# Kernel tuning notes

Hardware: AMD Instinct MI355X
Metric: run time of the kernel (lower is better)

## Reference

```python
import jax, jax.numpy as jnp
import numpy as np
import math


def setup_inputs() -> dict:
    key = jax.random.key(0)
    ks = jax.random.split(key, 8)
    B, L, d_model, d_state, d_conv, expand = 2, 512, 1024, 64, 4, 2
    d_inner = expand * d_model  # 2048
    x = jax.random.normal(ks[0], (B, L, d_model), jnp.float32)
    in_proj_w = jax.random.normal(ks[1], (d_model, 2 * d_inner), jnp.float32) * (d_model ** -0.5)
    conv_w = jax.random.normal(ks[2], (d_inner, 1, d_conv), jnp.float32) * (d_conv ** -0.5)
    conv_b = jnp.zeros((d_inner,), jnp.float32)
    x_proj_w = jax.random.normal(ks[3], (d_inner, 2 * d_state + 1), jnp.float32) * (d_inner ** -0.5)
    dt_w = jax.random.normal(ks[4], (1, d_inner), jnp.float32)
    # dt bias init: softplus^{-1} of dt ~ LogUniform(dt_min, dt_max)
    dt = jnp.exp(jax.random.uniform(ks[5], (d_inner,)) * (math.log(0.1) - math.log(0.001)) + math.log(0.001))
    dt_b = dt + jnp.log(-jnp.expm1(-dt))
    A_log = jnp.broadcast_to(jnp.log(jnp.arange(1, d_state + 1, dtype=jnp.float32)), (d_inner, d_state)) + 0.0
    D = jnp.ones((d_inner,), jnp.float32)
    out_proj_w = jax.random.normal(ks[6], (d_inner, d_model), jnp.float32) * (d_inner ** -0.5)
    return {"x": x, "in_proj_w": in_proj_w, "conv_w": conv_w, "conv_b": conv_b,
            "x_proj_w": x_proj_w, "dt_w": dt_w, "dt_b": dt_b, "A_log": A_log,
            "D": D, "out_proj_w": out_proj_w}


def _mamba_forward(x, in_proj_w, conv_w, conv_b, x_proj_w, dt_w, dt_b, A_log, D, out_proj_w):
    Bsz, L, _ = x.shape
    d_inner, _, K = conv_w.shape
    d_state = A_log.shape[1]
    # in_proj -> split into x-branch and gate z
    xz = x @ in_proj_w                       # (B, L, 2*d_inner)
    xs, z = jnp.split(xz, 2, axis=-1)
    # depthwise causal conv1d (pad K-1 on the left == torch pad both + truncate to L)
    xc = jax.lax.conv_general_dilated(
        xs.transpose(0, 2, 1), conv_w, (1,), [(K - 1, 0)],
        dimension_numbers=("NCH", "OIH", "NCH"), feature_group_count=d_inner)
    xc = xc + conv_b[None, :, None]
    xs = jax.nn.silu(xc.transpose(0, 2, 1))  # (B, L, d_inner)
    # input-dependent SSM params
    xp = xs @ x_proj_w                       # (B, L, 2*d_state + 1)
    Bm = xp[..., :d_state]                   # (B, L, N)
    Cm = xp[..., d_state:2 * d_state]        # (B, L, N)
    dt_raw = xp[..., -1:]                    # (B, L, 1)
    dt = jax.nn.softplus(dt_raw @ dt_w + dt_b)  # (B, L, d_inner)
    A = -jnp.exp(A_log)                      # (d_inner, N)

    def step(state, inp):
        x_t, B_t, C_t, dt_t = inp            # (B,d), (B,N), (B,N), (B,d)
        dA = jnp.exp(dt_t[..., None] * A)    # (B, d, N)
        state = dA * state + (dt_t * x_t)[..., None] * B_t[:, None, :]
        y = jnp.einsum("bdn,bn->bd", state, C_t) + D * x_t
        return state, y

    init = jnp.zeros((Bsz, d_inner, d_state), xs.dtype)
    seq = (xs.transpose(1, 0, 2), Bm.transpose(1, 0, 2),
           Cm.transpose(1, 0, 2), dt.transpose(1, 0, 2))
    new_state, ys = jax.lax.scan(step, init, seq)
    y = ys.transpose(1, 0, 2)                # (B, L, d_inner)
    y = y * jax.nn.silu(z)
    out = y @ out_proj_w                     # (B, L, d_model)
    return out, new_state


def reference(x, in_proj_w, conv_w, conv_b, x_proj_w, dt_w, dt_b, A_log, D, out_proj_w):
    return _mamba_forward(x, in_proj_w, conv_w, conv_b, x_proj_w, dt_w, dt_b, A_log, D, out_proj_w)
```

## Files before the change

kernel.cpp:

```cpp
#include <hip/hip_runtime.h>
#include <hip/hip_bf16.h>


#define N_TOK   1024
#define SEQ_L   512
#define D_MODEL 1024
#define D_INNER 2048
#define D_STATE 64
#define D_XZ    4096
#define N_XP    129

typedef __attribute__((ext_vector_type(8))) short bf16x8;
typedef __attribute__((ext_vector_type(4))) float f32x4;

__device__ __forceinline__ unsigned short f2bf(float f) {
  __hip_bfloat16 h = __float2bfloat16(f);
  return *reinterpret_cast<unsigned short*>(&h);
}
__device__ __forceinline__ float bf16lo(unsigned int u) { return __uint_as_float(u << 16); }
__device__ __forceinline__ float bf16hi(unsigned int u) { return __uint_as_float(u & 0xffff0000u); }

__global__ __launch_bounds__(256) void transpose_bf16(
    const float* __restrict__ src, __hip_bfloat16* __restrict__ dst, int R, int C) {
  __shared__ float t[64][65];
  int c0 = blockIdx.x * 64, r0 = blockIdx.y * 64;
  int tc = threadIdx.x & 63, tg = threadIdx.x >> 6;
#pragma unroll
  for (int i = 0; i < 16; ++i) {
    int r = r0 + tg + i * 4, c = c0 + tc;
    t[tg + i * 4][tc] = (r < R && c < C) ? src[(size_t)r * C + c] : 0.f;
  }
  __syncthreads();
#pragma unroll
  for (int i = 0; i < 16; ++i) {
    int c = c0 + tg + i * 4, r = r0 + tc;
    if (c < C && r < R) dst[(size_t)c * R + r] = __float2bfloat16(t[tc][tg + i * 4]);
  }
}

__global__ __launch_bounds__(256) void convert_bf16(
    const float* __restrict__ src, __hip_bfloat16* __restrict__ dst, int n) {
  int i = blockIdx.x * 256 + threadIdx.x;
  if (i < n) dst[i] = __float2bfloat16(src[i]);
}

template<int BM>
__global__ __launch_bounds__(256) void gemm_bf16_tn(
    const __hip_bfloat16* __restrict__ A, const __hip_bfloat16* __restrict__ Bt,
    float* __restrict__ C, int M, int N, int K) {
  const int MF = BM / 32;
  __shared__ short As[BM][40];
  __shared__ short Bs[128][40];
  const int brow = blockIdx.y * BM, bcol = blockIdx.x * 128;
  const int tid = threadIdx.x;
  const int lane = tid & 63, wave = tid >> 6;
  const int wm = wave >> 1, wn = wave & 1;
  const int l15 = lane & 15, lk = lane >> 4;
  f32x4 acc[MF][4] = {};
  for (int k0 = 0; k0 < K; k0 += 32) {
#pragma unroll
    for (int i = 0; i < BM / 64; ++i) {
      int v = tid + i * 256;
      int r = v >> 2, kc = (v & 3) * 8;
      *(bf16x8*)((char*)&As[0][0] + r * 80 + kc * 2) =
          *(const bf16x8*)&A[(size_t)(brow + r) * K + k0 + kc];
    }
#pragma unroll
    for (int i = 0; i < 2; ++i) {
      int v = tid + i * 256;
      int r = v >> 2, kc = (v & 3) * 8;
      *(bf16x8*)((char*)&Bs[0][0] + r * 80 + kc * 2) =
          *(const bf16x8*)&Bt[(size_t)(bcol + r) * K + k0 + kc];
    }
    __syncthreads();
    bf16x8 af[MF], bfr[4];
#pragma unroll
    for (int m = 0; m < MF; ++m)
      af[m] = *(const bf16x8*)((const char*)&As[0][0] + (wm * (BM / 2) + m * 16 + l15) * 80 + lk * 16);
#pragma unroll
    for (int n = 0; n < 4; ++n)
      bfr[n] = *(const bf16x8*)((const char*)&Bs[0][0] + (wn * 64 + n * 16 + l15) * 80 + lk * 16);
#pragma unroll
    for (int m = 0; m < MF; ++m)
#pragma unroll
      for (int n = 0; n < 4; ++n)
        acc[m][n] = __builtin_amdgcn_mfma_f32_16x16x32_bf16(af[m], bfr[n], acc[m][n], 0, 0, 0);
    __syncthreads();
  }
#pragma unroll
  for (int m = 0; m < MF; ++m) {
    int row = brow + wm * (BM / 2) + m * 16 + lk * 4;
#pragma unroll
    for (int n = 0; n < 4; ++n) {
      int col = bcol + wn * 64 + n * 16 + l15;
#pragma unroll
      for (int r = 0; r < 4; ++r)
        C[(size_t)(row + r) * N + col] = acc[m][n][r];
    }
  }
}

template<int BM>
__global__ __launch_bounds__(256) void gemm_splitk(
    const __hip_bfloat16* __restrict__ A, const __hip_bfloat16* __restrict__ Bt,
    float* __restrict__ P, int M, int N, int K, int kchunk) {
  const int MF = BM / 32;
  __shared__ short As[BM][40];
  __shared__ short Bs[128][40];
  const int brow = blockIdx.y * BM, bcol = blockIdx.x * 128;
  const int kbase = blockIdx.z * kchunk;
  const int tid = threadIdx.x;
  const int lane = tid & 63, wave = tid >> 6;
  const int wm = wave >> 1, wn = wave & 1;
  const int l15 = lane & 15, lk = lane >> 4;
  f32x4 acc[MF][4] = {};
  for (int k0 = kbase; k0 < kbase + kchunk; k0 += 32) {
#pragma unroll
    for (int i = 0; i < BM / 64; ++i) {
      int v = tid + i * 256;
      int r = v >> 2, kc = (v & 3) * 8;
      *(bf16x8*)((char*)&As[0][0] + r * 80 + kc * 2) =
          *(const bf16x8*)&A[(size_t)(brow + r) * K + k0 + kc];
    }
#pragma unroll
    for (int i = 0; i < 2; ++i) {
      int v = tid + i * 256;
      int r = v >> 2, kc = (v & 3) * 8;
      bf16x8 bv = {};
      if ((bcol + r) < N)
        bv = *(const bf16x8*)&Bt[(size_t)(bcol + r) * K + k0 + kc];
      *(bf16x8*)((char*)&Bs[0][0] + r * 80 + kc * 2) = bv;
    }
    __syncthreads();
    bf16x8 af[MF], bfr[4];
#pragma unroll
    for (int m = 0; m < MF; ++m)
      af[m] = *(const bf16x8*)((const char*)&As[0][0] + (wm * (BM / 2) + m * 16 + l15) * 80 + lk * 16);
#pragma unroll
    for (int n = 0; n < 4; ++n)
      bfr[n] = *(const bf16x8*)((const char*)&Bs[0][0] + (wn * 64 + n * 16 + l15) * 80 + lk * 16);
#pragma unroll
    for (int m = 0; m < MF; ++m)
#pragma unroll
      for (int n = 0; n < 4; ++n)
        acc[m][n] = __builtin_amdgcn_mfma_f32_16x16x32_bf16(af[m], bfr[n], acc[m][n], 0, 0, 0);
    __syncthreads();
  }
  float* Pz = P + (size_t)blockIdx.z * M * N;
#pragma unroll
  for (int m = 0; m < MF; ++m) {
    int row = brow + wm * (BM / 2) + m * 16 + lk * 4;
#pragma unroll
    for (int n = 0; n < 4; ++n) {
      int col = bcol + wn * 64 + n * 16 + l15;
      if (col < N) {
#pragma unroll
        for (int r = 0; r < 4; ++r)
          Pz[(size_t)(row + r) * N + col] = acc[m][n][r];
      }
    }
  }
}

template<int Z>
__global__ __launch_bounds__(256) void reduce_z(
    const float* __restrict__ P, float* __restrict__ out, int n) {
  int i = (blockIdx.x * 256 + threadIdx.x) * 4;
  if (i >= n) return;
  float4 s = *(const float4*)&P[i];
#pragma unroll
  for (int z = 1; z < Z; ++z) {
    float4 v = *(const float4*)&P[(size_t)z * n + i];
    s.x += v.x; s.y += v.y; s.z += v.z; s.w += v.w;
  }
  *(float4*)&out[i] = s;
}

__global__ __launch_bounds__(256) void reduce_bc(
    const float* __restrict__ P, float4* __restrict__ bcq,
    float* __restrict__ dtr) {
  int tok = blockIdx.x * 8 + (threadIdx.x >> 5);
  int ln = threadIdx.x & 31;
  const float* p0 = P + (size_t)tok * N_XP;
  float b0 = 0.f, b1 = 0.f, c0 = 0.f, c1 = 0.f;
#pragma unroll
  for (int z = 0; z < 16; ++z) {
    const float* pz = p0 + (size_t)z * N_TOK * N_XP;
    b0 += pz[ln]; b1 += pz[ln + 32];
    c0 += pz[64 + ln]; c1 += pz[64 + ln + 32];
  }
  bcq[(size_t)tok * 32 + ln] = make_float4(b0, b1, c0, c1);
  if (ln == 0) {
    float sd = 0.f;
    const float* pd = p0 + 128;
#pragma unroll
    for (int z = 0; z < 16; ++z) sd += pd[(size_t)z * N_TOK * N_XP];
    dtr[tok] = sd;
  }
}

__global__ __launch_bounds__(256) void conv_silu_kernel(
    const float* __restrict__ xz, const float* __restrict__ cw,
    const float* __restrict__ cb, float* __restrict__ xc,
    __hip_bfloat16* __restrict__ xcb) {
  int idx = blockIdx.x * 256 + threadIdx.x;
  int c = idx & (D_INNER - 1);
  int tok = idx >> 11;
  int l = tok & (SEQ_L - 1);
  float acc = cb[c];
#pragma unroll
  for (int k = 0; k < 4; ++k) {
    int ll = l - 3 + k;
    if (ll >= 0) acc = fmaf(xz[(size_t)(tok - 3 + k) * D_XZ + c], cw[c * 4 + k], acc);
  }
  float v = acc / (1.f + __expf(-acc));
  xc[idx] = v;
  xcb[idx] = __float2bfloat16(v);
}

__global__ __launch_bounds__(256) void pack_kernel(
    const float* __restrict__ xzf, const float* __restrict__ xc,
    const float* __restrict__ dtr, const float* __restrict__ dt_w,
    const float* __restrict__ dt_b, const float* __restrict__ Dv,
    float2* __restrict__ uaT, unsigned int* __restrict__ ug2) {
  __shared__ float2 la[64][33];
  int tok0 = blockIdx.x * 32, d0 = blockIdx.y * 64;
  int t = threadIdx.x;
  int dl = t & 63, tc = t >> 6;
  int d = d0 + dl;
  float w = dt_w[d], bb = dt_b[d], Dd = Dv[d];
#pragma unroll
  for (int p = 0; p < 8; ++p) {
    int tl = p * 4 + tc;
    int tok = tok0 + tl;
    float xt = xc[(size_t)tok * D_INNER + d];
    float z = xzf[(size_t)tok * D_XZ + D_INNER + d];
    float dt = dtr[tok] * w + bb;
    dt = (dt > 20.f) ? dt : log1pf(__expf(dt));
    la[dl][tl] = make_float2(dt, dt * xt);
    float g = z / (1.f + __expf(-z));
    ug2[(size_t)tok * D_INNER + d] =
        (unsigned int)f2bf(Dd * xt) | ((unsigned int)f2bf(g) << 16);
  }
  __syncthreads();
  int tl2 = t & 31, dg = t >> 5;
#pragma unroll
  for (int q = 0; q < 8; ++q) {
    int dl2 = q * 8 + dg;
    uaT[(size_t)(d0 + dl2) * N_TOK + tok0 + tl2] = la[dl2][tl2];
  }
}

__global__ __launch_bounds__(256) void gate_kernel(
    const float* __restrict__ praw, const unsigned int* __restrict__ ug2,
    __hip_bfloat16* __restrict__ ybb) {
  __shared__ float tile[64][65];
  int tok0 = blockIdx.x * 64, d0 = blockIdx.y * 64;
  int t = threadIdx.x, tc = t & 63, tg = t >> 6;
#pragma unroll
  for (int i = 0; i < 16; ++i) {
    int dl = tg + i * 4;
    tile[dl][tc] = praw[(size_t)(d0 + dl) * N_TOK + tok0 + tc];
  }
  __syncthreads();
#pragma unroll
  for (int i = 0; i < 16; ++i) {
    int tl = tg + i * 4;
    size_t idx = (size_t)(tok0 + tl) * D_INNER + d0 + tc;
    unsigned u = ug2[idx];
    float v = (tile[tc][tl] + bf16lo(u)) * bf16hi(u);
    ybb[idx] = __float2bfloat16(v);
  }
}

template<int CTRL>
__device__ __forceinline__ float dppadd(float v) {
  int t = __builtin_amdgcn_update_dpp(0, __float_as_int(v), CTRL, 0xF, 0xF, true);
  return v + __int_as_float(t);
}
__device__ __forceinline__ float wave_sum32(float v) {
  v = dppadd<0x111>(v);
  v = dppadd<0x112>(v);
  v = dppadd<0x114>(v);
  v = dppadd<0x118>(v);
  v = dppadd<0x142>(v);
  return v;
}

__global__ __launch_bounds__(256) void scan_fused(
    const float2* __restrict__ uaT, const float4* __restrict__ bcq,
    const float* __restrict__ A_log, float* __restrict__ praw,
    float* __restrict__ state_out) {
  __shared__ float lP[8][64], lS[8][64];
  int bd = blockIdx.x;
  int d = bd & (D_INNER - 1), b = bd >> 11;
  int tid = threadIdx.x;
  int wave = tid >> 6, lane = tid & 63;
  int h = lane >> 5, ln = lane & 31;
  int ch = wave * 2 + h;
  int n0 = ln, n1 = ln + 32;
  const float LOG2E = 1.4426950408889634f;
  float a2_0 = -__expf(A_log[d * D_STATE + n0]) * LOG2E;
  float a2_1 = -__expf(A_log[d * D_STATE + n1]) * LOG2E;
  int tok0 = b * SEQ_L + ch * 64;
  const float2* u0 = uaT + (size_t)d * N_TOK + tok0;
  const float4* q0 = bcq + (size_t)tok0 * 32 + ln;

  float s0 = 0.f, s1 = 0.f, P0 = 1.f, P1 = 1.f;
  {
    const float2* u = u0; const float4* q = q0;
#pragma unroll 1
    for (int t8 = 0; t8 < 8; ++t8) {
#pragma unroll
      for (int j = 0; j < 8; ++j) {
        float2 uv = u[j];
        float4 qv = q[j * 32];
        float dA0 = exp2f(uv.x * a2_0);
        float dA1 = exp2f(uv.x * a2_1);
        P0 *= dA0; P1 *= dA1;
        s0 = fmaf(dA0, s0, uv.y * qv.x);
        s1 = fmaf(dA1, s1, uv.y * qv.y);
      }
      u += 8; q += 256;
    }
  }
  lP[ch][n0] = P0; lP[ch][n1] = P1;
  lS[ch][n0] = s0; lS[ch][n1] = s1;
  __syncthreads();
  float si0 = 0.f, si1 = 0.f;
#pragma unroll
  for (int c = 0; c < 7; ++c) {
    if (c < ch) {
      si0 = fmaf(lP[c][n0], si0, lS[c][n0]);
      si1 = fmaf(lP[c][n1], si1, lS[c][n1]);
    }
  }
  if (ch == 7) {
    state_out[(size_t)bd * D_STATE + n0] = fmaf(P0, si0, s0);
    state_out[(size_t)bd * D_STATE + n1] = fmaf(P1, si1, s1);
  }

  s0 = si0; s1 = si1;
  {
    const float2* u = u0; const float4* q = q0;
    float* po = praw + (size_t)d * N_TOK + tok0;
#pragma unroll 1
    for (int t8 = 0; t8 < 8; ++t8) {
      float pb[8];
#pragma unroll
      for (int j = 0; j < 8; ++j) {
        float2 uv = u[j];
        float4 qv = q[j * 32];
        float dA0 = exp2f(uv.x * a2_0);
        float dA1 = exp2f(uv.x * a2_1);
        s0 = fmaf(dA0, s0, uv.y * qv.x);
        s1 = fmaf(dA1, s1, uv.y * qv.y);
        float p = s0 * qv.z;
        p = fmaf(s1, qv.w, p);
        pb[j] = wave_sum32(p);
      }
      if (ln == 31) {
        *(float4*)(po + t8 * 8) = make_float4(pb[0], pb[1], pb[2], pb[3]);
        *(float4*)(po + t8 * 8 + 4) = make_float4(pb[4], pb[5], pb[6], pb[7]);
      }
      u += 8; q += 256;
    }
  }
}

extern "C" void kernel_launch(void* const* d_in, const int* in_sizes, int n_in,
                              void* d_out, int out_size, void* d_ws, size_t ws_size,
                              hipStream_t stream) {
  const float* x         = (const float*)d_in[0];
  const float* in_proj_w = (const float*)d_in[1];
  const float* conv_w    = (const float*)d_in[2];
  const float* conv_b    = (const float*)d_in[3];
  const float* x_proj_w  = (const float*)d_in[4];
  const float* dt_w      = (const float*)d_in[5];
  const float* dt_b      = (const float*)d_in[6];
  const float* A_log     = (const float*)d_in[7];
  const float* Dvec      = (const float*)d_in[8];
  const float* out_proj_w= (const float*)d_in[9];

  char* w = (char*)d_ws;
  __hip_bfloat16* Wt1 = (__hip_bfloat16*)w; w += (size_t)D_XZ * D_MODEL * 2;
  __hip_bfloat16* Wt2 = (__hip_bfloat16*)w; w += (size_t)N_XP * D_INNER * 2;
  __hip_bfloat16* Wt3 = (__hip_bfloat16*)w; w += (size_t)D_MODEL * D_INNER * 2;
  __hip_bfloat16* xb  = (__hip_bfloat16*)w; w += (size_t)N_TOK * D_MODEL * 2;
  float*          xzf = (float*)w;          w += (size_t)N_TOK * D_XZ * 4;
  float*          xc  = (float*)w;          w += (size_t)N_TOK * D_INNER * 4;
  __hip_bfloat16* xcb = (__hip_bfloat16*)w; w += (size_t)N_TOK * D_INNER * 2;
  float*          P   = (float*)w;          w += (size_t)16 * N_TOK * N_XP * 4;
  float4*         bcq = (float4*)w;         w += (size_t)N_TOK * 32 * 16;
  float*          dtr = (float*)w;          w += (size_t)N_TOK * 4;
  float2*         uaT = (float2*)w;         w += (size_t)D_INNER * N_TOK * 8;
  unsigned int*   ug2 = (unsigned int*)w;   w += (size_t)N_TOK * D_INNER * 4;
  float*          praw = P;
  __hip_bfloat16* ybb  = xcb;
  float*          Pg   = xzf;

  float* out       = (float*)d_out;
  float* state_out = out + (size_t)N_TOK * D_MODEL;

  dim3 blk(256);
  transpose_bf16<<<dim3(D_XZ / 64, D_MODEL / 64), blk, 0, stream>>>(in_proj_w, Wt1, D_MODEL, D_XZ);
  transpose_bf16<<<dim3((N_XP + 63) / 64, D_INNER / 64), blk, 0, stream>>>(x_proj_w, Wt2, D_INNER, N_XP);
  transpose_bf16<<<dim3(D_MODEL / 64, D_INNER / 64), blk, 0, stream>>>(out_proj_w, Wt3, D_INNER, D_MODEL);
  convert_bf16<<<(N_TOK * D_MODEL) / 256, blk, 0, stream>>>(x, xb, N_TOK * D_MODEL);
  gemm_bf16_tn<64><<<dim3(D_XZ / 128, N_TOK / 64), blk, 0, stream>>>(xb, Wt1, xzf, N_TOK, D_XZ, D_MODEL);
  conv_silu_kernel<<<(N_TOK * D_INNER) / 256, blk, 0, stream>>>(xzf, conv_w, conv_b, xc, xcb);
  gemm_splitk<64><<<dim3((N_XP + 127) / 128, N_TOK / 64, 16), blk, 0, stream>>>(xcb, Wt2, P, N_TOK, N_XP, D_INNER, 128);
  reduce_bc<<<N_TOK / 8, blk, 0, stream>>>(P, bcq, dtr);
  pack_kernel<<<dim3(N_TOK / 32, D_INNER / 64), blk, 0, stream>>>(xzf, xc, dtr, dt_w, dt_b, Dvec, uaT, ug2);
  scan_fused<<<2 * D_INNER, blk, 0, stream>>>(uaT, bcq, A_log, praw, state_out);
  gate_kernel<<<dim3(N_TOK / 64, D_INNER / 64), blk, 0, stream>>>(praw, ug2, ybb);
  gemm_splitk<64><<<dim3(D_MODEL / 128, N_TOK / 64, 4), blk, 0, stream>>>(ybb, Wt3, Pg, N_TOK, D_MODEL, D_INNER, 512);
  reduce_z<4><<<(N_TOK * D_MODEL) / 1024, blk, 0, stream>>>(Pg, out, N_TOK * D_MODEL);
}
```

Measured before the change: 300.4 us.

## Fuse weight prep launches and split scan into 16 chunks of 16-lane groups

Merges the three weight transposes and the input bf16 conversion into one prep kernel, with vectorized conversion, to cut launch overhead. The scan is restructured so each thread owns four state elements and works in 16-lane groups, with 16 sequence chunks of 32 tokens per block instead of 8 chunks of 64. B and C are stored as separate float4 arrays to match the new lane layout. This halves the serial chunk length and shortens the per-token reduction to four DPP steps. In exchange it raises per-thread register use and lengthens the serial cross-chunk combine.

```diff
diff --git a/kernel.cpp b/kernel.cpp
--- a/kernel.cpp
+++ b/kernel.cpp
@@ -20,10 +20,30 @@
 __device__ __forceinline__ float bf16lo(unsigned int u) { return __uint_as_float(u << 16); }
 __device__ __forceinline__ float bf16hi(unsigned int u) { return __uint_as_float(u & 0xffff0000u); }
 
-__global__ __launch_bounds__(256) void transpose_bf16(
-    const float* __restrict__ src, __hip_bfloat16* __restrict__ dst, int R, int C) {
+__global__ __launch_bounds__(256) void prep_kernel(
+    const float* __restrict__ w1, const float* __restrict__ w2,
+    const float* __restrict__ w3, const float* __restrict__ x,
+    __hip_bfloat16* __restrict__ Wt1, __hip_bfloat16* __restrict__ Wt2,
+    __hip_bfloat16* __restrict__ Wt3, __hip_bfloat16* __restrict__ xb) {
+  int bid = blockIdx.x;
+  if (bid >= 1632) {
+    int base = (bid - 1632) * 16384 + threadIdx.x * 4;
+#pragma unroll
+    for (int p = 0; p < 16; ++p) {
+      int i = base + p * 1024;
+      float4 v = *(const float4*)&x[i];
+      unsigned lo = (unsigned)f2bf(v.x) | ((unsigned)f2bf(v.y) << 16);
+      unsigned hi = (unsigned)f2bf(v.z) | ((unsigned)f2bf(v.w) << 16);
+      *(uint2*)&xb[i] = make_uint2(lo, hi);
+    }
+    return;
+  }
   __shared__ float t[64][65];
-  int c0 = blockIdx.x * 64, r0 = blockIdx.y * 64;
+  const float* src; __hip_bfloat16* dst; int R, C, cx, t0;
+  if (bid < 1024)      { src = w1; dst = Wt1; R = D_MODEL; C = D_XZ;   cx = 64; t0 = bid; }
+  else if (bid < 1120) { src = w2; dst = Wt2; R = D_INNER; C = N_XP;   cx = 3;  t0 = bid - 1024; }
+  else                 { src = w3; dst = Wt3; R = D_INNER; C = D_MODEL; cx = 16; t0 = bid - 1120; }
+  int c0 = (t0 % cx) * 64, r0 = (t0 / cx) * 64;
   int tc = threadIdx.x & 63, tg = threadIdx.x >> 6;
 #pragma unroll
   for (int i = 0; i < 16; ++i) {
@@ -36,12 +56,6 @@
     int c = c0 + tg + i * 4, r = r0 + tc;
     if (c < C && r < R) dst[(size_t)c * R + r] = __float2bfloat16(t[tc][tg + i * 4]);
   }
-}
-
-__global__ __launch_bounds__(256) void convert_bf16(
-    const float* __restrict__ src, __hip_bfloat16* __restrict__ dst, int n) {
-  int i = blockIdx.x * 256 + threadIdx.x;
-  if (i < n) dst[i] = __float2bfloat16(src[i]);
 }
 
 template<int BM>
@@ -177,24 +191,24 @@
 }
 
 __global__ __launch_bounds__(256) void reduce_bc(
-    const float* __restrict__ P, float4* __restrict__ bcq,
-    float* __restrict__ dtr) {
-  int tok = blockIdx.x * 8 + (threadIdx.x >> 5);
-  int ln = threadIdx.x & 31;
+    const float* __restrict__ P, float4* __restrict__ Bq,
+    float4* __restrict__ Cq, float* __restrict__ dtr) {
+  int tok = blockIdx.x * 16 + (threadIdx.x >> 4);
+  int lq = threadIdx.x & 15;
   const float* p0 = P + (size_t)tok * N_XP;
-  float b0 = 0.f, b1 = 0.f, c0 = 0.f, c1 = 0.f;
+  float b0 = 0, b1 = 0, b2 = 0, b3 = 0, c0 = 0, c1 = 0, c2 = 0, c3 = 0;
 #pragma unroll
   for (int z = 0; z < 16; ++z) {
     const float* pz = p0 + (size_t)z * N_TOK * N_XP;
-    b0 += pz[ln]; b1 += pz[ln + 32];
-    c0 += pz[64 + ln]; c1 += pz[64 + ln + 32];
-  }
-  bcq[(size_t)tok * 32 + ln] = make_float4(b0, b1, c0, c1);
-  if (ln == 0) {
+    b0 += pz[lq];      b1 += pz[lq + 16]; b2 += pz[lq + 32]; b3 += pz[lq + 48];
+    c0 += pz[64 + lq]; c1 += pz[80 + lq]; c2 += pz[96 + lq]; c3 += pz[112 + lq];
+  }
+  Bq[(size_t)tok * 16 + lq] = make_float4(b0, b1, b2, b3);
+  Cq[(size_t)tok * 16 + lq] = make_float4(c0, c1, c2, c3);
+  if (lq == 0) {
     float sd = 0.f;
-    const float* pd = p0 + 128;
-#pragma unroll
-    for (int z = 0; z < 16; ++z) sd += pd[(size_t)z * N_TOK * N_XP];
+#pragma unroll
+    for (int z = 0; z < 16; ++z) sd += p0[(size_t)z * N_TOK * N_XP + 128];
     dtr[tok] = sd;
   }
 }
@@ -278,92 +292,104 @@
   int t = __builtin_amdgcn_update_dpp(0, __float_as_int(v), CTRL, 0xF, 0xF, true);
   return v + __int_as_float(t);
 }
-__device__ __forceinline__ float wave_sum32(float v) {
+__device__ __forceinline__ float qsum16(float v) {
   v = dppadd<0x111>(v);
   v = dppadd<0x112>(v);
   v = dppadd<0x114>(v);
   v = dppadd<0x118>(v);
-  v = dppadd<0x142>(v);
   return v;
 }
 
 __global__ __launch_bounds__(256) void scan_fused(
-    const float2* __restrict__ uaT, const float4* __restrict__ bcq,
-    const float* __restrict__ A_log, float* __restrict__ praw,
-    float* __restrict__ state_out) {
-  __shared__ float lP[8][64], lS[8][64];
+    const float2* __restrict__ uaT, const float4* __restrict__ Bq,
+    const float4* __restrict__ Cq, const float* __restrict__ A_log,
+    float* __restrict__ praw, float* __restrict__ state_out) {
+  __shared__ float lP[16][64], lS[16][64];
   int bd = blockIdx.x;
   int d = bd & (D_INNER - 1), b = bd >> 11;
   int tid = threadIdx.x;
   int wave = tid >> 6, lane = tid & 63;
-  int h = lane >> 5, ln = lane & 31;
-  int ch = wave * 2 + h;
-  int n0 = ln, n1 = ln + 32;
-  const float LOG2E = 1.4426950408889634f;
-  float a2_0 = -__expf(A_log[d * D_STATE + n0]) * LOG2E;
-  float a2_1 = -__expf(A_log[d * D_STATE + n1]) * LOG2E;
-  int tok0 = b * SEQ_L + ch * 64;
+  int qw = lane >> 4, lq = lane & 15;
+  int ch = wave * 4 + qw;
+  const float L2E = 1.4426950408889634f;
+  float a20 = -__expf(A_log[d * D_STATE + lq]) * L2E;
+  float a21 = -__expf(A_log[d * D_STATE + lq + 16]) * L2E;
+  float a22 = -__expf(A_log[d * D_STATE + lq + 32]) * L2E;
+  float a23 = -__expf(A_log[d * D_STATE + lq + 48]) * L2E;
+  int tok0 = b * SEQ_L + ch * 32;
   const float2* u0 = uaT + (size_t)d * N_TOK + tok0;
-  const float4* q0 = bcq + (size_t)tok0 * 32 + ln;
-
-  float s0 = 0.f, s1 = 0.f, P0 = 1.f, P1 = 1.f;
+  const float4* B0 = Bq + (size_t)tok0 * 16 + lq;
+  const float4* C0 = Cq + (size_t)tok0 * 16 + lq;
+
+  float s0 = 0, s1 = 0, s2 = 0, s3 = 0, P0 = 1, P1 = 1, P2 = 1, P3 = 1;
   {
-    const float2* u = u0; const float4* q = q0;
+    const float2* u = u0; const float4* pB = B0;
 #pragma unroll 1
-    for (int t8 = 0; t8 < 8; ++t8) {
+    for (int t8 = 0; t8 < 4; ++t8) {
 #pragma unroll
       for (int j = 0; j < 8; ++j) {
         float2 uv = u[j];
-        float4 qv = q[j * 32];
-        float dA0 = exp2f(uv.x * a2_0);
-        float dA1 = exp2f(uv.x * a2_1);
-        P0 *= dA0; P1 *= dA1;
-        s0 = fmaf(dA0, s0, uv.y * qv.x);
-        s1 = fmaf(dA1, s1, uv.y * qv.y);
+        float4 bv = pB[j * 16];
+        float e0 = exp2f(uv.x * a20), e1 = exp2f(uv.x * a21);
+        float e2 = exp2f(uv.x * a22), e3 = exp2f(uv.x * a23);
+        P0 *= e0; P1 *= e1; P2 *= e2; P3 *= e3;
+        s0 = fmaf(e0, s0, uv.y * bv.x);
+        s1 = fmaf(e1, s1, uv.y * bv.y);
+        s2 = fmaf(e2, s2, uv.y * bv.z);
+        s3 = fmaf(e3, s3, uv.y * bv.w);
       }
-      u += 8; q += 256;
-    }
-  }
-  lP[ch][n0] = P0; lP[ch][n1] = P1;
-  lS[ch][n0] = s0; lS[ch][n1] = s1;
+      u += 8; pB += 128;
+    }
+  }
+  lP[ch][lq] = P0; lP[ch][lq + 16] = P1; lP[ch][lq + 32] = P2; lP[ch][lq + 48] = P3;
+  lS[ch][lq] = s0; lS[ch][lq + 16] = s1; lS[ch][lq + 32] = s2; lS[ch][lq + 48] = s3;
   __syncthreads();
-  float si0 = 0.f, si1 = 0.f;
-#pragma unroll
-  for (int c = 0; c < 7; ++c) {
+  float si0 = 0, si1 = 0, si2 = 0, si3 = 0;
+#pragma unroll
+  for (int c = 0; c < 15; ++c) {
     if (c < ch) {
-      si0 = fmaf(lP[c][n0], si0, lS[c][n0]);
-      si1 = fmaf(lP[c][n1], si1, lS[c][n1]);
-    }
-  }
-  if (ch == 7) {
-    state_out[(size_t)bd * D_STATE + n0] = fmaf(P0, si0, s0);
-    state_out[(size_t)bd * D_STATE + n1] = fmaf(P1, si1, s1);
-  }
-
-  s0 = si0; s1 = si1;
+      si0 = fmaf(lP[c][lq], si0, lS[c][lq]);
+      si1 = fmaf(lP[c][lq + 16], si1, lS[c][lq + 16]);
+      si2 = fmaf(lP[c][lq + 32], si2, lS[c][lq + 32]);
+      si3 = fmaf(lP[c][lq + 48], si3, lS[c][lq + 48]);
+    }
+  }
+  if (ch == 15) {
+    state_out[(size_t)bd * D_STATE + lq]      = fmaf(P0, si0, s0);
+    state_out[(size_t)bd * D_STATE + lq + 16] = fmaf(P1, si1, s1);
+    state_out[(size_t)bd * D_STATE + lq + 32] = fmaf(P2, si2, s2);
+    state_out[(size_t)bd * D_STATE + lq + 48] = fmaf(P3, si3, s3);
+  }
+
+  s0 = si0; s1 = si1; s2 = si2; s3 = si3;
   {
-    const float2* u = u0; const float4* q = q0;
+    const float2* u = u0; const float4* pB = B0; const float4* pC = C0;
     float* po = praw + (size_t)d * N_TOK + tok0;
 #pragma unroll 1
-    for (int t8 = 0; t8 < 8; ++t8) {
+    for (int t8 = 0; t8 < 4; ++t8) {
       float pb[8];
 #pragma unroll
       for (int j = 0; j < 8; ++j) {
         float2 uv = u[j];
-        float4 qv = q[j * 32];
-        float dA0 = exp2f(uv.x * a2_0);
-        float dA1 = exp2f(uv.x * a2_1);
-        s0 = fmaf(dA0, s0, uv.y * qv.x);
-        s1 = fmaf(dA1, s1, uv.y * qv.y);
-        float p = s0 * qv.z;
-        p = fmaf(s1, qv.w, p);
-        pb[j] = wave_sum32(p);
+        float4 bv = pB[j * 16];
+        float4 cv = pC[j * 16];
+        float e0 = exp2f(uv.x * a20), e1 = exp2f(uv.x * a21);
+        float e2 = exp2f(uv.x * a22), e3 = exp2f(uv.x * a23);
+        s0 = fmaf(e0, s0, uv.y * bv.x);
+        s1 = fmaf(e1, s1, uv.y * bv.y);
+        s2 = fmaf(e2, s2, uv.y * bv.z);
+        s3 = fmaf(e3, s3, uv.y * bv.w);
+        float p = s0 * cv.x;
+        p = fmaf(s1, cv.y, p);
+        p = fmaf(s2, cv.z, p);
+        p = fmaf(s3, cv.w, p);
+        pb[j] = qsum16(p);
       }
-      if (ln == 31) {
+      if (lq == 15) {
         *(float4*)(po + t8 * 8) = make_float4(pb[0], pb[1], pb[2], pb[3]);
         *(float4*)(po + t8 * 8 + 4) = make_float4(pb[4], pb[5], pb[6], pb[7]);
       }
-      u += 8; q += 256;
+      u += 8; pB += 128; pC += 128;
     }
   }
 }
@@ -391,7 +417,8 @@
   float*          xc  = (float*)w;          w += (size_t)N_TOK * D_INNER * 4;
   __hip_bfloat16* xcb = (__hip_bfloat16*)w; w += (size_t)N_TOK * D_INNER * 2;
   float*          P   = (float*)w;          w += (size_t)16 * N_TOK * N_XP * 4;
-  float4*         bcq = (float4*)w;         w += (size_t)N_TOK * 32 * 16;
+  float4*         Bq  = (float4*)w;         w += (size_t)N_TOK * 16 * 16;
+  float4*         Cq  = (float4*)w;         w += (size_t)N_TOK * 16 * 16;
   float*          dtr = (float*)w;          w += (size_t)N_TOK * 4;
   float2*         uaT = (float2*)w;         w += (size_t)D_INNER * N_TOK * 8;
   unsigned int*   ug2 = (unsigned int*)w;   w += (size_t)N_TOK * D_INNER * 4;
@@ -403,16 +430,14 @@
   float* state_out = out + (size_t)N_TOK * D_MODEL;
 
   dim3 blk(256);
-  transpose_bf16<<<dim3(D_XZ / 64, D_MODEL / 64), blk, 0, stream>>>(in_proj_w, Wt1, D_MODEL, D_XZ);
-  transpose_bf16<<<dim3((N_XP + 63) / 64, D_INNER / 64), blk, 0, stream>>>(x_proj_w, Wt2, D_INNER, N_XP);
-  transpose_bf16<<<dim3(D_MODEL / 64, D_INNER / 64), blk, 0, stream>>>(out_proj_w, Wt3, D_INNER, D_MODEL);
-  convert_bf16<<<(N_TOK * D_MODEL) / 256, blk, 0, stream>>>(x, xb, N_TOK * D_MODEL);
+  prep_kernel<<<1696, blk, 0, stream>>>(in_proj_w, x_proj_w, out_proj_w, x,
+                                        Wt1, Wt2, Wt3, xb);
   gemm_bf16_tn<64><<<dim3(D_XZ / 128, N_TOK / 64), blk, 0, stream>>>(xb, Wt1, xzf, N_TOK, D_XZ, D_MODEL);
   conv_silu_kernel<<<(N_TOK * D_INNER) / 256, blk, 0, stream>>>(xzf, conv_w, conv_b, xc, xcb);
   gemm_splitk<64><<<dim3((N_XP + 127) / 128, N_TOK / 64, 16), blk, 0, stream>>>(xcb, Wt2, P, N_TOK, N_XP, D_INNER, 128);
-  reduce_bc<<<N_TOK / 8, blk, 0, stream>>>(P, bcq, dtr);
+  reduce_bc<<<N_TOK / 16, blk, 0, stream>>>(P, Bq, Cq, dtr);
   pack_kernel<<<dim3(N_TOK / 32, D_INNER / 64), blk, 0, stream>>>(xzf, xc, dtr, dt_w, dt_b, Dvec, uaT, ug2);
-  scan_fused<<<2 * D_INNER, blk, 0, stream>>>(uaT, bcq, A_log, praw, state_out);
+  scan_fused<<<2 * D_INNER, blk, 0, stream>>>(uaT, Bq, Cq, A_log, praw, state_out);
   gate_kernel<<<dim3(N_TOK / 64, D_INNER / 64), blk, 0, stream>>>(praw, ug2, ybb);
   gemm_splitk<64><<<dim3(D_MODEL / 128, N_TOK / 64, 4), blk, 0, stream>>>(ybb, Wt3, Pg, N_TOK, D_MODEL, D_INNER, 512);
   reduce_z<4><<<(N_TOK * D_MODEL) / 1024, blk, 0, stream>>>(Pg, out, N_TOK * D_MODEL);
```

After: 270.1 us. -10.1%, faster.
